# Kernel tuning notes

Measured on AMD Instinct MI355X. Metric: run time of the kernel, lower is better.

Reference implementation:

```python
import jax, jax.numpy as jnp
import numpy as np

B, L, HID = 2, 2048, 2048
N_HEAD, HEAD_DIM, N_KV = 32, 64, 8
N_Q_PER_KV = N_HEAD // N_KV  # 4
SCALE = 0.125  # 1/sqrt(HEAD_DIM)
PAD_START = L - 256  # last 256 key positions are padding
NEG = -1e9


def setup_inputs() -> dict:
    key = jax.random.key(0)
    ks = jax.random.split(key, 8)
    query = jax.random.normal(ks[0], (B, L, HID), jnp.float32)
    kv = jax.random.normal(ks[1], (B, L, HID), jnp.float32)
    # additive causal mask (0 on/below diagonal, -1e9 above)
    i = jnp.arange(L)
    attn_mask = jnp.where(i[None, :] > i[:, None], NEG, 0.0).astype(jnp.float32)
    # key padding mask: True == padded position
    key_padding_mask = (i[None, :] >= PAD_START) & jnp.ones((B, 1), bool)
    s = 0.02
    Wq = jax.random.normal(ks[2], (HID, N_HEAD * HEAD_DIM), jnp.float32) * s
    bq = jnp.zeros((N_HEAD * HEAD_DIM,), jnp.float32)
    Wkv = jax.random.normal(ks[3], (HID, 2 * N_KV * HEAD_DIM), jnp.float32) * s
    bkv = jnp.zeros((2 * N_KV * HEAD_DIM,), jnp.float32)
    Wo = jax.random.normal(ks[4], (N_HEAD * HEAD_DIM, HID), jnp.float32) * s
    bo = jnp.zeros((HID,), jnp.float32)
    return {"query": query, "kv": kv, "Wq": Wq, "bq": bq, "Wkv": Wkv,
            "bkv": bkv, "Wo": Wo, "bo": bo, "attn_mask": attn_mask,
            "key_padding_mask": key_padding_mask}


def reference(query, kv, Wq, bq, Wkv, bkv, Wo, bo, attn_mask, key_padding_mask):
    b, l, _ = query.shape
    q = (query @ Wq + bq).reshape(b, l, N_HEAD, HEAD_DIM).transpose(0, 2, 1, 3)  # [B,H,L,D]
    kvp = kv @ Wkv + bkv                                   # [B,L,2*NKV*D]
    k, v = jnp.split(kvp, 2, axis=-1)
    k = k.reshape(b, l, N_KV, HEAD_DIM)
    v = v.reshape(b, l, N_KV, HEAD_DIM)
    # GQA: repeat_interleave KV heads to match Q heads
    k = jnp.repeat(k, N_Q_PER_KV, axis=2).transpose(0, 2, 1, 3)  # [B,H,L,D]
    v = jnp.repeat(v, N_Q_PER_KV, axis=2).transpose(0, 2, 1, 3)
    qk = jnp.einsum('bhqd,bhkd->bhqk', q, k) * SCALE
    qk = qk + attn_mask                                     # additive mask
    qk = jnp.where(key_padding_mask[:, None, None, :], NEG, qk)
    p = jax.nn.softmax(qk.astype(jnp.float32), axis=-1).astype(q.dtype)
    attn = jnp.einsum('bhqk,bhkd->bhqd', p, v)
    attn = attn.transpose(0, 2, 1, 3).reshape(b, l, N_HEAD * HEAD_DIM)
    out = attn @ Wo + bo
    return out
```

## Files before the change

kernel.cpp:

```cpp
#include <hip/hip_runtime.h>
#include <stdint.h>

#define L_SEQ 2048
#define HID 2048
#define PADK 1792
#define QSCALE 0.18033688011112042f

typedef unsigned short us_t;
typedef __attribute__((ext_vector_type(8))) short bf16x8;
typedef __attribute__((ext_vector_type(4))) float f32x4;

__device__ __forceinline__ float bf2f(us_t u) {
    union { unsigned int i; float f; } c; c.i = ((unsigned int)u) << 16; return c.f;
}
__device__ __forceinline__ us_t f2bf(float f) {
    union { float f; unsigned int i; } c; c.f = f;
    unsigned int i = c.i;
    return (us_t)((i + 0x7FFFu + ((i >> 16) & 1u)) >> 16);
}
__device__ __forceinline__ unsigned int pk_bf16(float a, float b) {
#if __has_builtin(__builtin_amdgcn_cvt_pk_bf16_f32)
    auto r = __builtin_amdgcn_cvt_pk_bf16_f32(a, b);
    unsigned int u; __builtin_memcpy(&u, &r, 4); return u;
#else
    return (unsigned int)f2bf(a) | ((unsigned int)f2bf(b) << 16);
#endif
}
__device__ __forceinline__ float fast_exp2(float x) {
#if __has_builtin(__builtin_amdgcn_exp2f)
    return __builtin_amdgcn_exp2f(x);
#else
    return exp2f(x);
#endif
}
__device__ __forceinline__ void gload_lds16(const us_t* g, us_t* l) {
    __builtin_amdgcn_global_load_lds((const __attribute__((address_space(1))) void*)g,
                                     (__attribute__((address_space(3))) void*)l, 16, 0, 0);
}
__device__ __forceinline__ int detect_bf16(const unsigned int* q) {
    __shared__ int sc[4];
    unsigned int v = q[threadIdx.x & 255];
    unsigned int e = (v >> 7) & 0xFFu;
    unsigned long long bb = __ballot(e >= 112u && e <= 133u);
    int cnt = __popcll(bb);
    if ((threadIdx.x & 63) == 0) sc[threadIdx.x >> 6] = cnt;
    __syncthreads();
    return (sc[0] + sc[1] + sc[2] + sc[3]) > 128;
}
__device__ __forceinline__ int detect_bf16_512(const unsigned int* q) {
    __shared__ int sc[8];
    unsigned int v = q[threadIdx.x & 255];
    unsigned int e = (v >> 7) & 0xFFu;
    unsigned long long bb = __ballot(e >= 112u && e <= 133u);
    int cnt = __popcll(bb);
    if ((threadIdx.x & 63) == 0) sc[threadIdx.x >> 6] = cnt;
    __syncthreads();
    int s = 0;
    #pragma unroll
    for (int i = 0; i < 8; ++i) s += sc[i];
    return s > 256;
}

__global__ __launch_bounds__(256) void prep(const unsigned int* __restrict__ qdet,
                                            const void* __restrict__ query,
                                            const void* __restrict__ kvsrc,
                                            const void* __restrict__ Wq,
                                            const void* __restrict__ Wkv,
                                            const void* __restrict__ Wo,
                                            us_t* __restrict__ Aq, us_t* __restrict__ Akv,
                                            us_t* __restrict__ Wqt, us_t* __restrict__ Wkvt,
                                            us_t* __restrict__ Wot) {
    __shared__ us_t tile[64][65];
    const int bf = detect_bf16(qdet);
    int id = blockIdx.x;
    if (id < 8192) {
        const void* s = (id < 4096) ? query : kvsrc;
        us_t* d       = (id < 4096) ? Aq : Akv;
        int cid = (id & 4095) * 256 + threadIdx.x;
        if (bf) {
            ((bf16x8*)d)[cid] = ((const bf16x8*)s)[cid];
        } else {
            const float* sp = (const float*)s + (size_t)cid * 8;
            f32x4 a = *(const f32x4*)sp, b2 = *(const f32x4*)(sp + 4);
            union { bf16x8 v; unsigned int dw[4]; } o;
            o.dw[0] = pk_bf16(a[0], a[1]);   o.dw[1] = pk_bf16(a[2], a[3]);
            o.dw[2] = pk_bf16(b2[0], b2[1]); o.dw[3] = pk_bf16(b2[2], b2[3]);
            ((bf16x8*)d)[cid] = o.v;
        }
        return;
    }
    id -= 8192;
    const void* s; us_t* d; int R, C, bx, by;
    if (id < 1024)      { s = Wq;  d = Wqt;  R = 2048; C = 2048; bx = id & 31; by = id >> 5; }
    else if (id < 1536) { id -= 1024; s = Wkv; d = Wkvt; R = 2048; C = 1024; bx = id & 15; by = id >> 4; }
    else                { id -= 1536; s = Wo;  d = Wot;  R = 2048; C = 2048; bx = id & 31; by = id >> 5; }
    const int c0 = bx * 64, r0 = by * 64;
    #pragma unroll
    for (int i = 0; i < 16; ++i) {
        int idx = threadIdx.x + i * 256;
        int r = idx >> 6, c = idx & 63;
        tile[r][c] = bf ? ((const us_t*)s)[(size_t)(r0 + r) * C + c0 + c]
                        : f2bf(((const float*)s)[(size_t)(r0 + r) * C + c0 + c]);
    }
    __syncthreads();
    #pragma unroll
    for (int i = 0; i < 16; ++i) {
        int idx = threadIdx.x + i * 256;
        int c = idx >> 6, r = idx & 63;
        d[(size_t)(c0 + c) * R + r0 + r] = tile[r][c];
    }
}

template<int MH, int NH, bool RDA, bool RDB, typename STG, typename TAIL>
__device__ __forceinline__ void phase8(const us_t* Ab, const us_t* Bb,
                                       int wm, int wn, int l15, int cs0, int cs1,
                                       bf16x8 (&af)[4][2], bf16x8 (&bf)[2][2],
                                       f32x4 (&acc)[8][4], STG&& stg, TAIL&& tail) {
    if (RDA) {
        #pragma unroll
        for (int mt = 0; mt < 4; ++mt) {
            const us_t* p = &Ab[(wm * 128 + MH * 64 + mt * 16 + l15) * 64];
            af[mt][0] = *(const bf16x8*)&p[cs0 * 8];
            af[mt][1] = *(const bf16x8*)&p[cs1 * 8];
        }
    }
    if (RDB) {
        #pragma unroll
        for (int nt = 0; nt < 2; ++nt) {
            const us_t* p = &Bb[(wn * 64 + NH * 32 + nt * 16 + l15) * 64];
            bf[nt][0] = *(const bf16x8*)&p[cs0 * 8];
            bf[nt][1] = *(const bf16x8*)&p[cs1 * 8];
        }
    }
    stg();
    if (RDA && RDB) asm volatile("s_waitcnt lgkmcnt(8)" ::: "memory");
    __builtin_amdgcn_s_barrier();
    asm volatile("s_waitcnt lgkmcnt(0)" ::: "memory");
    __builtin_amdgcn_sched_barrier(0);
    __builtin_amdgcn_s_setprio(1);
    #pragma unroll
    for (int ki = 0; ki < 2; ++ki)
        #pragma unroll
        for (int mt = 0; mt < 4; ++mt)
            #pragma unroll
            for (int nt = 0; nt < 2; ++nt)
                acc[MH * 4 + mt][NH * 2 + nt] = __builtin_amdgcn_mfma_f32_16x16x32_bf16(
                    af[mt][ki], bf[nt][ki], acc[MH * 4 + mt][NH * 2 + nt], 0, 0, 0);
    __builtin_amdgcn_s_setprio(0);
    tail();
    __builtin_amdgcn_s_barrier();
}

__device__ __forceinline__ void gemm256(const us_t* __restrict__ Ag,
                                        const us_t* __restrict__ Bg,
                                        int bm, int bn, us_t* sh,
                                        f32x4 (&acc)[8][4]) {
    us_t* As0 = sh;           us_t* As1 = sh + 16384;
    us_t* Bs0 = sh + 32768;   us_t* Bs1 = sh + 49152;
    const int t = threadIdx.x;
    const int w = t >> 6, lane = t & 63, l15 = lane & 15, quad = lane >> 4;
    const int wm = w >> 2, wn = w & 3;
    const int cs0 = quad ^ (l15 & 7);
    const int cs1 = (4 + quad) ^ (l15 & 7);

    int aoff[2][2], boff[2][2], adst[2][2], bdst[2][2];
    #pragma unroll
    for (int u = 0; u < 2; ++u)
        #pragma unroll
        for (int j = 0; j < 2; ++j) {
            int row0 = j * 128 + u * 64 + w * 8;
            int row  = row0 + (lane >> 3);
            int col  = ((lane & 7) ^ (row & 7)) * 8;
            aoff[u][j] = (bm + row) * 2048 + col;
            adst[u][j] = row0 * 64;
            int ci   = w * 2 + j;
            int rb0  = (ci >> 2) * 64 + u * 32 + (ci & 3) * 8;
            int rowb = rb0 + (lane >> 3);
            int colb = ((lane & 7) ^ (rowb & 7)) * 8;
            boff[u][j] = (bn + rowb) * 2048 + colb;
            bdst[u][j] = rb0 * 64;
        }

#define STAGE_A(U, KT, DST) do { \
        gload_lds16(Ag + (size_t)aoff[U][0] + (KT) * 64, (DST) + adst[U][0]); \
        gload_lds16(Ag + (size_t)aoff[U][1] + (KT) * 64, (DST) + adst[U][1]); } while (0)
#define STAGE_B(U, KT, DST) do { \
        gload_lds16(Bg + (size_t)boff[U][0] + (KT) * 64, (DST) + bdst[U][0]); \
        gload_lds16(Bg + (size_t)boff[U][1] + (KT) * 64, (DST) + bdst[U][1]); } while (0)

    #pragma unroll
    for (int i = 0; i < 8; ++i)
        #pragma unroll
        for (int j = 0; j < 4; ++j) acc[i][j] = (f32x4){0.f, 0.f, 0.f, 0.f};

    STAGE_A(0, 0, As0); STAGE_B(0, 0, Bs0);
    STAGE_A(1, 0, As0); STAGE_B(1, 0, Bs0);
    STAGE_A(0, 1, As1); STAGE_B(0, 1, Bs1);
    asm volatile("s_waitcnt vmcnt(4)" ::: "memory");
    __builtin_amdgcn_s_barrier();

    bf16x8 af[4][2], blo[2][2], bhi[2][2];
    auto notail = [] {};
    #pragma unroll 1
    for (int it = 0; it < 16; ++it) {
        const bool more = (it < 15);
        const int t1 = 2 * it + 1, t2 = 2 * it + 2, t3 = 2 * it + 3;
        phase8<0, 0, true,  true >(As0, Bs0, wm, wn, l15, cs0, cs1, af, blo, acc,
            [&] { STAGE_A(1, t1, As1); }, notail);
        phase8<0, 1, false, true >(As0, Bs0, wm, wn, l15, cs0, cs1, af, bhi, acc,
            [&] { STAGE_B(1, t1, Bs1); }, notail);
        phase8<1, 0, true,  false>(As0, Bs0, wm, wn, l15, cs0, cs1, af, blo, acc,
            [&] { if (more) STAGE_A(0, t2, As0); }, notail);
        phase8<1, 1, false, false>(As0, Bs0, wm, wn, l15, cs0, cs1, af, bhi, acc,
            [&] { if (more) STAGE_B(0, t2, Bs0); },
            [&] { if (more) asm volatile("s_waitcnt vmcnt(4)" ::: "memory");
                  else      asm volatile("s_waitcnt vmcnt(0)" ::: "memory"); });
        phase8<0, 0, true,  true >(As1, Bs1, wm, wn, l15, cs0, cs1, af, blo, acc,
            [&] { if (more) STAGE_A(1, t2, As0); }, notail);
        phase8<0, 1, false, true >(As1, Bs1, wm, wn, l15, cs0, cs1, af, bhi, acc,
            [&] { if (more) STAGE_B(1, t2, Bs0); }, notail);
        phase8<1, 0, true,  false>(As1, Bs1, wm, wn, l15, cs0, cs1, af, blo, acc,
            [&] { if (more) STAGE_A(0, t3, As1); }, notail);
        phase8<1, 1, false, false>(As1, Bs1, wm, wn, l15, cs0, cs1, af, bhi, acc,
            [&] { if (more) STAGE_B(0, t3, Bs1); },
            [&] { if (more) asm volatile("s_waitcnt vmcnt(4)" ::: "memory");
                  else      asm volatile("s_waitcnt vmcnt(0)" ::: "memory"); });
    }
#undef STAGE_A
#undef STAGE_B
}

__global__ __launch_bounds__(512, 2) void qkv_gemm(const unsigned int* __restrict__ qdet,
                                                   const us_t* __restrict__ Aq,
                                                   const us_t* __restrict__ Akv,
                                                   const us_t* __restrict__ Wqt,
                                                   const us_t* __restrict__ Wkvt,
                                                   const void* __restrict__ bq,
                                                   const void* __restrict__ bkv,
                                                   us_t* __restrict__ Qm,
                                                   us_t* __restrict__ Km,
                                                   us_t* __restrict__ Vg) {
    __shared__ us_t sh[65536];
    const int bf = detect_bf16_512(qdet);
    const int t = threadIdx.x;
    const int w = t >> 6, lane = t & 63, l15 = lane & 15, quad = lane >> 4;
    const int wm = w >> 2, wn = w & 3;

    int id = blockIdx.x;
    const us_t* Ag; const us_t* Bg; int bm, bn; bool isQ;
    if (id < 128) { isQ = true;  Ag = Aq;  Bg = Wqt;  bm = (id >> 3) * 256; bn = (id & 7) * 256; }
    else { id -= 128; isQ = false; Ag = Akv; Bg = Wkvt; bm = (id >> 2) * 256; bn = (id & 3) * 256; }

    f32x4 acc[8][4];
    gemm256(Ag, Bg, bm, bn, sh, acc);

    if (isQ) {
        #pragma unroll
        for (int an = 0; an < 4; ++an) {
            int col = bn + wn * 64 + an * 16 + l15;
            float bvv = bf ? bf2f(((const us_t*)bq)[col]) : ((const float*)bq)[col];
            #pragma unroll
            for (int am = 0; am < 8; ++am)
                #pragma unroll
                for (int r = 0; r < 4; ++r) {
                    int row = bm + wm * 128 + am * 16 + quad * 4 + r;
                    Qm[(size_t)row * 2048 + col] = f2bf((acc[am][an][r] + bvv) * QSCALE);
                }
        }
    } else if (bn < 512) {
        #pragma unroll
        for (int an = 0; an < 4; ++an) {
            int col = bn + wn * 64 + an * 16 + l15;
            float bvv = bf ? bf2f(((const us_t*)bkv)[col]) : ((const float*)bkv)[col];
            #pragma unroll
            for (int am = 0; am < 8; ++am)
                #pragma unroll
                for (int r = 0; r < 4; ++r) {
                    int row = bm + wm * 128 + am * 16 + quad * 4 + r;
                    Km[(size_t)row * 512 + col] = f2bf(acc[am][an][r] + bvv);
                }
        }
    } else {
        const int b2 = bm >> 11, tok0 = bm & 2047;
        #pragma unroll
        for (int half = 0; half < 2; ++half) {
            __syncthreads();
            if ((wn >> 1) == half) {
                #pragma unroll
                for (int an = 0; an < 4; ++an) {
                    int col = bn + wn * 64 + an * 16 + l15;
                    float bvv = bf ? bf2f(((const us_t*)bkv)[col]) : ((const float*)bkv)[col];
                    int cl = (wn & 1) * 64 + an * 16 + l15;
                    #pragma unroll
                    for (int am = 0; am < 8; ++am)
                        #pragma unroll
                        for (int r = 0; r < 4; ++r) {
                            int tok = wm * 128 + am * 16 + quad * 4 + r;
                            sh[cl * 258 + tok] = f2bf(acc[am][an][r] + bvv);
                        }
                }
            }
            __syncthreads();
            size_t vrow0 = (size_t)(b2 * 512 + (bn - 512) + half * 128);
            #pragma unroll
            for (int jj = 0; jj < 8; ++jj) {
                int idx = t + jj * 512;
                int c2 = idx >> 5, ch = idx & 31;
                bf16x8 vv = *(const bf16x8*)&sh[c2 * 258 + ch * 8];
                *(bf16x8*)(Vg + (vrow0 + c2) * (size_t)2048 + tok0 + ch * 8) = vv;
            }
        }
    }
}

__device__ __forceinline__ void gemm_core(const us_t* __restrict__ A,
                                          const us_t* __restrict__ Bt,
                                          int K, int bm, int bn, int t,
                                          us_t (&As)[2][8192], us_t (&Bs)[2][8192],
                                          f32x4 (&acc)[4][4]) {
    const int w = t >> 6, lane = t & 63, l15 = lane & 15, quad = lane >> 4;
    const int wm = (w & 1) * 64, wn = (w >> 1) * 64;
    int rA[4], cA[4];
    #pragma unroll
    for (int i = 0; i < 4; ++i) {
        int p = (w * 4 + i) * 64 + lane;
        int row = p >> 3, cs = p & 7;
        rA[i] = row; cA[i] = (cs ^ (row & 7)) * 8;
    }
    #pragma unroll
    for (int i = 0; i < 4; ++i) {
        gload_lds16(A  + (size_t)(bm + rA[i]) * K + cA[i], &As[0][(w * 4 + i) * 512]);
        gload_lds16(Bt + (size_t)(bn + rA[i]) * K + cA[i], &Bs[0][(w * 4 + i) * 512]);
    }
    int pb = 0;
    for (int k0 = 0; k0 < K; k0 += 64) {
        __syncthreads();
        if (k0 + 64 < K) {
            #pragma unroll
            for (int i = 0; i < 4; ++i) {
                gload_lds16(A  + (size_t)(bm + rA[i]) * K + k0 + 64 + cA[i], &As[pb ^ 1][(w * 4 + i) * 512]);
                gload_lds16(Bt + (size_t)(bn + rA[i]) * K + k0 + 64 + cA[i], &Bs[pb ^ 1][(w * 4 + i) * 512]);
            }
        }
        #pragma unroll
        for (int ki = 0; ki < 2; ++ki) {
            bf16x8 af[4], bfr[4];
            #pragma unroll
            for (int mt = 0; mt < 4; ++mt) {
                int row = wm + mt * 16 + l15;
                int cs  = (ki * 4 + quad) ^ (row & 7);
                af[mt] = *(const bf16x8*)&As[pb][row * 64 + cs * 8];
            }
            #pragma unroll
            for (int nt = 0; nt < 4; ++nt) {
                int row = wn + nt * 16 + l15;
                int cs  = (ki * 4 + quad) ^ (row & 7);
                bfr[nt] = *(const bf16x8*)&Bs[pb][row * 64 + cs * 8];
            }
            #pragma unroll
            for (int mt = 0; mt < 4; ++mt)
                #pragma unroll
                for (int nt = 0; nt < 4; ++nt)
                    acc[mt][nt] = __builtin_amdgcn_mfma_f32_16x16x32_bf16(af[mt], bfr[nt], acc[mt][nt], 0, 0, 0);
        }
        pb ^= 1;
    }
}

__global__ __launch_bounds__(256, 2) void o_gemm(const unsigned int* __restrict__ qdet,
                                                 const us_t* __restrict__ Ao,
                                                 const us_t* __restrict__ Wot,
                                                 const void* __restrict__ bo,
                                                 void* __restrict__ Out) {
    __shared__ us_t As[2][8192], Bs[2][8192];
    const int bf = detect_bf16(qdet);
    const int t = threadIdx.x;
    const int w = t >> 6, lane = t & 63, l15 = lane & 15, quad = lane >> 4;
    const int wm = (w & 1) * 64, wn = (w >> 1) * 64;
    const int bm = blockIdx.y * 128, bn = blockIdx.x * 128;
    f32x4 acc[4][4];
    #pragma unroll
    for (int i = 0; i < 4; ++i)
        #pragma unroll
        for (int j = 0; j < 4; ++j) acc[i][j] = (f32x4){0.f, 0.f, 0.f, 0.f};
    gemm_core(Ao, Wot, 2048, bm, bn, t, As, Bs, acc);
    #pragma unroll
    for (int nt = 0; nt < 4; ++nt) {
        int col = bn + wn + nt * 16 + l15;
        float bvv = bf ? bf2f(((const us_t*)bo)[col]) : ((const float*)bo)[col];
        #pragma unroll
        for (int mt = 0; mt < 4; ++mt)
            #pragma unroll
            for (int r = 0; r < 4; ++r) {
                int row = bm + wm + mt * 16 + quad * 4 + r;
                float v = acc[mt][nt][r] + bvv;
                if (bf) ((us_t*)Out)[(size_t)row * 2048 + col] = f2bf(v);
                else    ((float*)Out)[(size_t)row * 2048 + col] = v;
            }
    }
}

__device__ __forceinline__ void qk_exp(const bf16x8 kb[2][4], const bf16x8 qf[2][2],
                                       int q0, int k0, int l15, int quad,
                                       bf16x8 pa[2][2]) {
    f32x4 sa[2][4];
    #pragma unroll
    for (int mt = 0; mt < 2; ++mt)
        #pragma unroll
        for (int nt = 0; nt < 4; ++nt) sa[mt][nt] = (f32x4){0.f, 0.f, 0.f, 0.f};
    #pragma unroll
    for (int ki = 0; ki < 2; ++ki)
        #pragma unroll
        for (int mt = 0; mt < 2; ++mt)
            #pragma unroll
            for (int nt = 0; nt < 4; ++nt)
                sa[mt][nt] = __builtin_amdgcn_mfma_f32_16x16x32_bf16(kb[ki][nt], qf[mt][ki], sa[mt][nt], 0, 0, 0);
    const bool nm = (k0 + 63 > q0);
    #pragma unroll
    for (int mt = 0; mt < 2; ++mt) {
        const int qrow = q0 + mt * 16 + l15;
        union { bf16x8 v; unsigned int dw[4]; } u;
        #pragma unroll
        for (int k2 = 0; k2 < 2; ++k2) {
            #pragma unroll
            for (int hf = 0; hf < 2; ++hf) {
                const int nt = k2 * 2 + hf;
                const int keyb = k0 + k2 * 32 + hf * 4 + quad * 8;
                float e[4];
                #pragma unroll
                for (int r = 0; r < 4; ++r) {
                    float s = sa[mt][nt][r];
                    if (nm && (keyb + r > qrow)) s = -1e30f;
                    e[r] = fast_exp2(s);
                }
                u.dw[hf * 2]     = pk_bf16(e[0], e[1]);
                u.dw[hf * 2 + 1] = pk_bf16(e[2], e[3]);
            }
            pa[mt][k2] = u.v;
        }
    }
}

__global__ __launch_bounds__(256, 2) void attn_mfma(const us_t* __restrict__ Q,
                                                    const us_t* __restrict__ Km,
                                                    const us_t* __restrict__ Vg,
                                                    us_t* __restrict__ Am) {
    __shared__ us_t Ks[2][4096];
    __shared__ us_t Vt[2][4096];

    const int bid = blockIdx.x;
    const int pr  = bid & 31;
    const int kvh = (bid >> 5) & 7;
    const int b   = bid >> 8;
    const int t = threadIdx.x, w = t >> 6, lane = t & 63, l15 = lane & 15, quad = lane >> 4;
    const int h = kvh * 4 + w;
    const int q0h = 2016 - 32 * pr, q0l = 32 * pr;
    const int kend0 = min(q0h + 32, PADK), kend1 = min(q0l + 32, PADK);

    bf16x8 ones;
    #pragma unroll
    for (int j = 0; j < 8; ++j) ones[j] = (short)0x3F80;

    const us_t* Kbase = Km + (size_t)(b * L_SEQ) * 512 + kvh * 64;
    const us_t* Vbase = Vg + (size_t)(b * 512 + kvh * 64) * L_SEQ;

    size_t ksrc[2], vsrc[2];
    #pragma unroll
    for (int i = 0; i < 2; ++i) {
        int idx = (w * 2 + i) * 64 + lane;
        int p = idx >> 3, cs = idx & 7, c = cs ^ (p & 7);
        int gk = (p & 0x23) | ((p & 0x0C) << 1) | ((p & 0x10) >> 2);
        ksrc[i] = (size_t)gk * 512 + c * 8;
        vsrc[i] = (size_t)p * 2048 + c * 8;
    }

    bf16x8 qfh[2][2], qfl[2][2];
    #pragma unroll
    for (int mt = 0; mt < 2; ++mt)
        #pragma unroll
        for (int ki = 0; ki < 2; ++ki) {
            qfh[mt][ki] = *(const bf16x8*)(Q + (size_t)(b * L_SEQ + q0h + mt * 16 + l15) * HID
                                             + h * 64 + ki * 32 + quad * 8);
            qfl[mt][ki] = *(const bf16x8*)(Q + (size_t)(b * L_SEQ + q0l + mt * 16 + l15) * HID
                                             + h * 64 + ki * 32 + quad * 8);
        }

    f32x4 oah[2][4], oal[2][4], lah[2], lal[2];
    #pragma unroll
    for (int mt = 0; mt < 2; ++mt) {
        lah[mt] = (f32x4){0.f, 0.f, 0.f, 0.f};
        lal[mt] = (f32x4){0.f, 0.f, 0.f, 0.f};
        #pragma unroll
        for (int dn = 0; dn < 4; ++dn) {
            oah[mt][dn] = (f32x4){0.f, 0.f, 0.f, 0.f};
            oal[mt][dn] = (f32x4){0.f, 0.f, 0.f, 0.f};
        }
    }

    #pragma unroll
    for (int i = 0; i < 2; ++i) {
        gload_lds16(Kbase + ksrc[i], &Ks[0][(w * 2 + i) * 512]);
        gload_lds16(Vbase + vsrc[i], &Vt[0][(w * 2 + i) * 512]);
    }

    int pb = 0;
    for (int k0 = 0; k0 < kend0; k0 += 64) {
        __syncthreads();
        if (k0 + 64 < kend0) {
            #pragma unroll
            for (int i = 0; i < 2; ++i) {
                gload_lds16(Kbase + (size_t)(k0 + 64) * 512 + ksrc[i], &Ks[pb ^ 1][(w * 2 + i) * 512]);
                gload_lds16(Vbase + (k0 + 64) + vsrc[i],               &Vt[pb ^ 1][(w * 2 + i) * 512]);
            }
        }
        const bool dolight = (k0 < kend1);

        bf16x8 kb[2][4];
        #pragma unroll
        for (int ki = 0; ki < 2; ++ki)
            #pragma unroll
            for (int nt = 0; nt < 4; ++nt) {
                int row = nt * 16 + l15;
                int cs  = (ki * 4 + quad) ^ (row & 7);
                kb[ki][nt] = *(const bf16x8*)&Ks[pb][row * 64 + cs * 8];
            }

        bf16x8 pah[2][2], pal[2][2];
        qk_exp(kb, qfh, q0h, k0, l15, quad, pah);
        if (dolight) qk_exp(kb, qfl, q0l, k0, l15, quad, pal);

        bf16x8 vb[2][4];
        #pragma unroll
        for (int k2 = 0; k2 < 2; ++k2)
            #pragma unroll
            for (int dn = 0; dn < 4; ++dn) {
                int d  = dn * 16 + l15;
                int cs = (k2 * 4 + quad) ^ (d & 7);
                vb[k2][dn] = *(const bf16x8*)&Vt[pb][d * 64 + cs * 8];
            }

        #pragma unroll
        for (int k2 = 0; k2 < 2; ++k2)
            #pragma unroll
            for (int mt = 0; mt < 2; ++mt) {
                lah[mt] = __builtin_amdgcn_mfma_f32_16x16x32_bf16(pah[mt][k2], ones, lah[mt], 0, 0, 0);
                #pragma unroll
                for (int dn = 0; dn < 4; ++dn)
                    oah[mt][dn] = __builtin_amdgcn_mfma_f32_16x16x32_bf16(pah[mt][k2], vb[k2][dn], oah[mt][dn], 0, 0, 0);
            }
        if (dolight) {
            #pragma unroll
            for (int k2 = 0; k2 < 2; ++k2)
                #pragma unroll
                for (int mt = 0; mt < 2; ++mt) {
                    lal[mt] = __builtin_amdgcn_mfma_f32_16x16x32_bf16(pal[mt][k2], ones, lal[mt], 0, 0, 0);
                    #pragma unroll
                    for (int dn = 0; dn < 4; ++dn)
                        oal[mt][dn] = __builtin_amdgcn_mfma_f32_16x16x32_bf16(pal[mt][k2], vb[k2][dn], oal[mt][dn], 0, 0, 0);
                }
        }
        pb ^= 1;
    }

    #pragma unroll
    for (int mt = 0; mt < 2; ++mt)
        #pragma unroll
        for (int r = 0; r < 4; ++r) {
            float invh = 1.0f / lah[mt][r];
            float invl = 1.0f / lal[mt][r];
            int rowh = q0h + mt * 16 + quad * 4 + r;
            int rowl = q0l + mt * 16 + quad * 4 + r;
            #pragma unroll
            for (int dn = 0; dn < 4; ++dn) {
                Am[(size_t)(b * L_SEQ + rowh) * HID + h * 64 + dn * 16 + l15] =
                    f2bf(oah[mt][dn][r] * invh);
                Am[(size_t)(b * L_SEQ + rowl) * HID + h * 64 + dn * 16 + l15] =
                    f2bf(oal[mt][dn][r] * invl);
            }
        }
}

extern "C" void kernel_launch(void* const* d_in, const int* in_sizes, int n_in,
                              void* d_out, int out_size, void* d_ws, size_t ws_size,
                              hipStream_t stream) {
    const void* query = d_in[0];
    const void* kv    = d_in[1];
    const void* Wq    = d_in[2];
    const void* bq    = d_in[3];
    const void* Wkv   = d_in[4];
    const void* bkv   = d_in[5];
    const void* Wo    = d_in[6];
    const void* bo    = d_in[7];
    const unsigned int* qdet = (const unsigned int*)query;

    char* p = (char*)d_ws;
    us_t* Qm   = (us_t*)p;                p += (size_t)4096 * 2048 * 2;
    us_t* Km   = (us_t*)p;                p += (size_t)4096 * 512 * 2;
    us_t* Vg   = (us_t*)p;                p += (size_t)1024 * 2048 * 2;
    us_t* AqAm = (us_t*)p;                p += (size_t)4096 * 2048 * 2;
    us_t* Akv  = (us_t*)p;                p += (size_t)4096 * 2048 * 2;
    us_t* Wqt  = (us_t*)p;                p += (size_t)2048 * 2048 * 2;
    us_t* Wkvt = (us_t*)p;                p += (size_t)1024 * 2048 * 2;
    us_t* Wot  = (us_t*)p;

    dim3 blk(256);
    prep<<<dim3(10752), blk, 0, stream>>>(qdet, query, kv, Wq, Wkv, Wo,
                                          AqAm, Akv, Wqt, Wkvt, Wot);
    qkv_gemm<<<dim3(192), dim3(512), 0, stream>>>(qdet, AqAm, Akv, Wqt, Wkvt, bq, bkv,
                                                  Qm, Km, Vg);
    attn_mfma<<<dim3(512), blk, 0, stream>>>(Qm, Km, Vg, AqAm);
    o_gemm<<<dim3(16, 32), blk, 0, stream>>>(qdet, AqAm, Wot, bo, d_out);
}
```

Baseline: 360.2 us.

## Replace QKV GEMM phased pipeline with triple-buffered K=32 loop and remap blocks

Replaces the 8-phase double-buffered K=64 main loop of the 256x256 QKV GEMM with a simpler loop over K=32 slices. It uses a three-stage LDS ring, a single barrier per iteration and a prefetch two tiles ahead. LDS use per block shrinks from 128KB to 96KB, and the XOR swizzle changes to a 4-way pattern. Block IDs are also permuted so that blocks landing on the same XCD share operand rows for better L2 locality. The tradeoff is 64 iterations of barriers and waits instead of 16, and the interleaving of MFMAs with LDS reads is coarser.

```diff
diff --git a/kernel.cpp b/kernel.cpp
--- a/kernel.cpp
+++ b/kernel.cpp
@@ -111,123 +111,68 @@
     }
 }
 
-template<int MH, int NH, bool RDA, bool RDB, typename STG, typename TAIL>
-__device__ __forceinline__ void phase8(const us_t* Ab, const us_t* Bb,
-                                       int wm, int wn, int l15, int cs0, int cs1,
-                                       bf16x8 (&af)[4][2], bf16x8 (&bf)[2][2],
-                                       f32x4 (&acc)[8][4], STG&& stg, TAIL&& tail) {
-    if (RDA) {
-        #pragma unroll
-        for (int mt = 0; mt < 4; ++mt) {
-            const us_t* p = &Ab[(wm * 128 + MH * 64 + mt * 16 + l15) * 64];
-            af[mt][0] = *(const bf16x8*)&p[cs0 * 8];
-            af[mt][1] = *(const bf16x8*)&p[cs1 * 8];
-        }
-    }
-    if (RDB) {
-        #pragma unroll
-        for (int nt = 0; nt < 2; ++nt) {
-            const us_t* p = &Bb[(wn * 64 + NH * 32 + nt * 16 + l15) * 64];
-            bf[nt][0] = *(const bf16x8*)&p[cs0 * 8];
-            bf[nt][1] = *(const bf16x8*)&p[cs1 * 8];
-        }
-    }
-    stg();
-    if (RDA && RDB) asm volatile("s_waitcnt lgkmcnt(8)" ::: "memory");
-    __builtin_amdgcn_s_barrier();
-    asm volatile("s_waitcnt lgkmcnt(0)" ::: "memory");
-    __builtin_amdgcn_sched_barrier(0);
-    __builtin_amdgcn_s_setprio(1);
-    #pragma unroll
-    for (int ki = 0; ki < 2; ++ki)
-        #pragma unroll
-        for (int mt = 0; mt < 4; ++mt)
-            #pragma unroll
-            for (int nt = 0; nt < 2; ++nt)
-                acc[MH * 4 + mt][NH * 2 + nt] = __builtin_amdgcn_mfma_f32_16x16x32_bf16(
-                    af[mt][ki], bf[nt][ki], acc[MH * 4 + mt][NH * 2 + nt], 0, 0, 0);
-    __builtin_amdgcn_s_setprio(0);
-    tail();
-    __builtin_amdgcn_s_barrier();
-}
-
 __device__ __forceinline__ void gemm256(const us_t* __restrict__ Ag,
                                         const us_t* __restrict__ Bg,
                                         int bm, int bn, us_t* sh,
                                         f32x4 (&acc)[8][4]) {
-    us_t* As0 = sh;           us_t* As1 = sh + 16384;
-    us_t* Bs0 = sh + 32768;   us_t* Bs1 = sh + 49152;
     const int t = threadIdx.x;
     const int w = t >> 6, lane = t & 63, l15 = lane & 15, quad = lane >> 4;
     const int wm = w >> 2, wn = w & 3;
-    const int cs0 = quad ^ (l15 & 7);
-    const int cs1 = (4 + quad) ^ (l15 & 7);
-
-    int aoff[2][2], boff[2][2], adst[2][2], bdst[2][2];
-    #pragma unroll
-    for (int u = 0; u < 2; ++u)
-        #pragma unroll
-        for (int j = 0; j < 2; ++j) {
-            int row0 = j * 128 + u * 64 + w * 8;
-            int row  = row0 + (lane >> 3);
-            int col  = ((lane & 7) ^ (row & 7)) * 8;
-            aoff[u][j] = (bm + row) * 2048 + col;
-            adst[u][j] = row0 * 64;
-            int ci   = w * 2 + j;
-            int rb0  = (ci >> 2) * 64 + u * 32 + (ci & 3) * 8;
-            int rowb = rb0 + (lane >> 3);
-            int colb = ((lane & 7) ^ (rowb & 7)) * 8;
-            boff[u][j] = (bn + rowb) * 2048 + colb;
-            bdst[u][j] = rb0 * 64;
-        }
-
-#define STAGE_A(U, KT, DST) do { \
-        gload_lds16(Ag + (size_t)aoff[U][0] + (KT) * 64, (DST) + adst[U][0]); \
-        gload_lds16(Ag + (size_t)aoff[U][1] + (KT) * 64, (DST) + adst[U][1]); } while (0)
-#define STAGE_B(U, KT, DST) do { \
-        gload_lds16(Bg + (size_t)boff[U][0] + (KT) * 64, (DST) + bdst[U][0]); \
-        gload_lds16(Bg + (size_t)boff[U][1] + (KT) * 64, (DST) + bdst[U][1]); } while (0)
+    const int csA = (quad ^ (l15 & 3)) * 8;
+
+    int aoffs[2], boffs[2], slot[2];
+    #pragma unroll
+    for (int j = 0; j < 2; ++j) {
+        int row = (w * 2 + j) * 16 + (lane >> 2);
+        int col = ((lane & 3) ^ (row & 3)) * 8;
+        aoffs[j] = (bm + row) * 2048 + col;
+        boffs[j] = (bn + row) * 2048 + col;
+        slot[j]  = (w * 2 + j) * 512;
+    }
+
+#define STAGE(T, ABUF, BBUF) do { int k0_ = (T) * 32; \
+        gload_lds16(Ag + (size_t)(aoffs[0] + k0_), (ABUF) + slot[0]); \
+        gload_lds16(Ag + (size_t)(aoffs[1] + k0_), (ABUF) + slot[1]); \
+        gload_lds16(Bg + (size_t)(boffs[0] + k0_), (BBUF) + slot[0]); \
+        gload_lds16(Bg + (size_t)(boffs[1] + k0_), (BBUF) + slot[1]); } while (0)
 
     #pragma unroll
     for (int i = 0; i < 8; ++i)
         #pragma unroll
         for (int j = 0; j < 4; ++j) acc[i][j] = (f32x4){0.f, 0.f, 0.f, 0.f};
 
-    STAGE_A(0, 0, As0); STAGE_B(0, 0, Bs0);
-    STAGE_A(1, 0, As0); STAGE_B(1, 0, Bs0);
-    STAGE_A(0, 1, As1); STAGE_B(0, 1, Bs1);
+    STAGE(0, sh,        sh + 24576);
+    STAGE(1, sh + 8192, sh + 24576 + 8192);
     asm volatile("s_waitcnt vmcnt(4)" ::: "memory");
-    __builtin_amdgcn_s_barrier();
-
-    bf16x8 af[4][2], blo[2][2], bhi[2][2];
-    auto notail = [] {};
+
+    int cur = 0, nx = 2;
     #pragma unroll 1
-    for (int it = 0; it < 16; ++it) {
-        const bool more = (it < 15);
-        const int t1 = 2 * it + 1, t2 = 2 * it + 2, t3 = 2 * it + 3;
-        phase8<0, 0, true,  true >(As0, Bs0, wm, wn, l15, cs0, cs1, af, blo, acc,
-            [&] { STAGE_A(1, t1, As1); }, notail);
-        phase8<0, 1, false, true >(As0, Bs0, wm, wn, l15, cs0, cs1, af, bhi, acc,
-            [&] { STAGE_B(1, t1, Bs1); }, notail);
-        phase8<1, 0, true,  false>(As0, Bs0, wm, wn, l15, cs0, cs1, af, blo, acc,
-            [&] { if (more) STAGE_A(0, t2, As0); }, notail);
-        phase8<1, 1, false, false>(As0, Bs0, wm, wn, l15, cs0, cs1, af, bhi, acc,
-            [&] { if (more) STAGE_B(0, t2, Bs0); },
-            [&] { if (more) asm volatile("s_waitcnt vmcnt(4)" ::: "memory");
-                  else      asm volatile("s_waitcnt vmcnt(0)" ::: "memory"); });
-        phase8<0, 0, true,  true >(As1, Bs1, wm, wn, l15, cs0, cs1, af, blo, acc,
-            [&] { if (more) STAGE_A(1, t2, As0); }, notail);
-        phase8<0, 1, false, true >(As1, Bs1, wm, wn, l15, cs0, cs1, af, bhi, acc,
-            [&] { if (more) STAGE_B(1, t2, Bs0); }, notail);
-        phase8<1, 0, true,  false>(As1, Bs1, wm, wn, l15, cs0, cs1, af, blo, acc,
-            [&] { if (more) STAGE_A(0, t3, As1); }, notail);
-        phase8<1, 1, false, false>(As1, Bs1, wm, wn, l15, cs0, cs1, af, bhi, acc,
-            [&] { if (more) STAGE_B(0, t3, Bs1); },
-            [&] { if (more) asm volatile("s_waitcnt vmcnt(4)" ::: "memory");
-                  else      asm volatile("s_waitcnt vmcnt(0)" ::: "memory"); });
-    }
-#undef STAGE_A
-#undef STAGE_B
+    for (int it = 0; it < 64; ++it) {
+        const us_t* Ab = sh + cur * 8192;
+        const us_t* Bb = sh + 24576 + cur * 8192;
+        __builtin_amdgcn_s_barrier();
+        if (it + 2 < 64)
+            STAGE(it + 2, sh + nx * 8192, sh + 24576 + nx * 8192);
+
+        bf16x8 af[8], bv[4];
+        #pragma unroll
+        for (int mt = 0; mt < 8; ++mt)
+            af[mt] = *(const bf16x8*)&Ab[(wm * 128 + mt * 16 + l15) * 32 + csA];
+        #pragma unroll
+        for (int nt = 0; nt < 4; ++nt)
+            bv[nt] = *(const bf16x8*)&Bb[(wn * 64 + nt * 16 + l15) * 32 + csA];
+        #pragma unroll
+        for (int mt = 0; mt < 8; ++mt)
+            #pragma unroll
+            for (int nt = 0; nt < 4; ++nt)
+                acc[mt][nt] = __builtin_amdgcn_mfma_f32_16x16x32_bf16(af[mt], bv[nt], acc[mt][nt], 0, 0, 0);
+
+        if (it + 2 < 64) asm volatile("s_waitcnt vmcnt(4)" ::: "memory");
+        else             asm volatile("s_waitcnt vmcnt(0)" ::: "memory");
+        cur = (cur == 2) ? 0 : cur + 1;
+        nx  = (nx  == 2) ? 0 : nx + 1;
+    }
+#undef STAGE
 }
 
 __global__ __launch_bounds__(512, 2) void qkv_gemm(const unsigned int* __restrict__ qdet,
@@ -240,13 +185,14 @@
                                                    us_t* __restrict__ Qm,
                                                    us_t* __restrict__ Km,
                                                    us_t* __restrict__ Vg) {
-    __shared__ us_t sh[65536];
+    __shared__ us_t sh[49152];
     const int bf = detect_bf16_512(qdet);
     const int t = threadIdx.x;
     const int w = t >> 6, lane = t & 63, l15 = lane & 15, quad = lane >> 4;
     const int wm = w >> 2, wn = w & 3;
 
-    int id = blockIdx.x;
+    int bid = blockIdx.x;
+    int id = (bid & 7) * 24 + (bid >> 3);
     const us_t* Ag; const us_t* Bg; int bm, bn; bool isQ;
     if (id < 128) { isQ = true;  Ag = Aq;  Bg = Wqt;  bm = (id >> 3) * 256; bn = (id & 7) * 256; }
     else { id -= 128; isQ = false; Ag = Akv; Bg = Wkvt; bm = (id >> 2) * 256; bn = (id & 3) * 256; }
```

Result: slower. 376.7 us (+4.6%).
